# Kernel optimization log

Measured on AMD Instinct MI355X. Metric: run time of the kernel, lower is better.

The kernel has to match this reference:

```python
import jax, jax.numpy as jnp
import numpy as np

B, S, H, E = 8, 512, 1024, 8
T = B * S            # total tokens
CAP = T // E         # capacity, capacity_factor = 1.0


def _moe(x, wg, ew1, eb1, ew2, eb2):
    # x: [T, H] tokens; top-1 gating with capacity, DeepSpeed-style dispatch/combine
    gates = jax.nn.softmax(x @ wg)                      # [T, E]
    idx = jnp.argmax(gates, axis=-1)                    # [T]
    mask1 = jax.nn.one_hot(idx, E, dtype=x.dtype)       # [T, E]
    locations = jnp.cumsum(mask1, axis=0) - 1.0         # position within expert queue
    mask1 = mask1 * (locations < CAP).astype(x.dtype)   # drop overflow tokens
    gates1 = jnp.sum(gates * mask1, axis=-1)            # [T] combine weight
    locs = jnp.sum(locations * mask1, axis=-1).astype(jnp.int32)  # [T]
    loc_oh = jax.nn.one_hot(locs, CAP, dtype=x.dtype)   # [T, C]
    combine = gates1[:, None, None] * mask1[:, :, None] * loc_oh[:, None, :]  # [T,E,C]
    dispatch = (combine > 0).astype(x.dtype)            # [T, E, C]
    xd = jnp.einsum('sec,sm->ecm', dispatch, x)         # gather tokens per expert
    h = jnp.einsum('ecm,emn->ecn', xd, ew1) + eb1[:, None, :]
    h = jnp.einsum('ecn,enp->ecp', h, ew2) + eb2[:, None, :]
    return jnp.einsum('sec,ecm->sm', combine, h)        # scatter back, weighted


def setup_inputs() -> dict:
    key = jax.random.key(0)
    ks = jax.random.split(key, 16)
    w = lambda k, shape: jax.random.normal(k, shape, jnp.float32) * 0.02
    return {
        'x': jax.random.normal(ks[0], (B, S, H), jnp.float32),
        'y': jax.random.randint(ks[1], (B,), 0, H),
        'w1': w(ks[2], (H, H)), 'b1': jnp.zeros((H,), jnp.float32),
        'w2': w(ks[3], (H, H)), 'b2': jnp.zeros((H,), jnp.float32),
        'w3': w(ks[4], (H, H)), 'b3': jnp.zeros((H,), jnp.float32),
        'wg1': w(ks[5], (H, E)),
        'e1_w1': w(ks[6], (E, H, H)), 'e1_b1': jnp.zeros((E, H), jnp.float32),
        'e1_w2': w(ks[7], (E, H, H)), 'e1_b2': jnp.zeros((E, H), jnp.float32),
        'wg2': w(ks[8], (H, E)),
        'e2_w1': w(ks[9], (E, H, H)), 'e2_b1': jnp.zeros((E, H), jnp.float32),
        'e2_w2': w(ks[10], (E, H, H)), 'e2_b2': jnp.zeros((E, H), jnp.float32),
    }


def reference(x, y, w1, b1, w2, b2, w3, b3, wg1, e1_w1, e1_b1, e1_w2, e1_b2,
              wg2, e2_w1, e2_b1, e2_w2, e2_b2):
    xf = x.reshape(-1, H)                               # [T, H]
    hidden = xf @ w1 + b1
    out = _moe(hidden, wg1, e1_w1, e1_b1, e1_w2, e1_b2)
    out = out @ w2 + b2
    out = _moe(out, wg2, e2_w1, e2_b1, e2_w2, e2_b2)
    out = out @ w3 + b3
    hidden = hidden + out
    sent = hidden.reshape(B, S, H).mean(axis=1)         # [B, H] logits
    logp = jax.nn.log_softmax(sent, axis=-1)
    return -jnp.mean(logp[jnp.arange(B), y])
```

## Files before the change

### kernel.cpp

```cpp
#include <hip/hip_runtime.h>

#define TOK 4096
#define HID 1024
#define NEXP 8
#define CAP 512
#define WSZ 1048576

typedef _Float16 f16;
typedef f16 f16x8 __attribute__((ext_vector_type(8)));
typedef f16 f16x4 __attribute__((ext_vector_type(4)));
typedef f16 f16x2 __attribute__((ext_vector_type(2)));
typedef float f32x4 __attribute__((ext_vector_type(4)));

typedef const __attribute__((address_space(1))) void gvoid;
typedef __attribute__((address_space(3))) void lvoid;

__device__ __forceinline__ void gld16(const void* g, void* l) {
  __builtin_amdgcn_global_load_lds((gvoid*)g, (lvoid*)l, 16, 0, 0);
}

template<int MODE>
__global__ __launch_bounds__(512, 1) void gemm_h(
    const f16* __restrict__ A, const f16* __restrict__ Bt,
    const float* __restrict__ bias, f16* __restrict__ C,
    const int* __restrict__ rowmap, const float* __restrict__ gmax,
    int rowsPerExpert, long bStride, int biasStride)
{
  __shared__ f16 As[2][128 * 64];
  __shared__ f16 Bs[2][128 * 64];
  const int tid = threadIdx.x;
  const int w = tid >> 6, l = tid & 63;
  const int wr = w >> 2, wc = w & 3;

  const int orig = blockIdx.x;
  const int sw = (orig & 7) * 32 + (orig >> 3);
  const int bx = sw & 7, by = sw >> 3;
  const int e = (by * 128) / rowsPerExpert;

  const int lr = l >> 3;
  const int chunkSw = ((l & 7) ^ lr) * 8;

  const f16* pst[4];
  if (w < 4) {
    #pragma unroll
    for (int i = 0; i < 4; ++i) {
      int r = by * 128 + w * 32 + i * 8 + lr;
      long tok = r;
      if (MODE == 1) { int t = rowmap[r]; tok = (t < 0) ? (long)TOK : (long)t; }
      pst[i] = A + tok * HID + chunkSw;
    }
  } else {
    #pragma unroll
    for (int i = 0; i < 4; ++i)
      pst[i] = Bt + (size_t)e * bStride
             + (size_t)(bx * 128 + (w - 4) * 32 + i * 8 + lr) * HID + chunkSw;
  }

  f32x4 acc[4][2];
  #pragma unroll
  for (int i = 0; i < 4; ++i)
    #pragma unroll
    for (int j = 0; j < 2; ++j) acc[i][j] = (f32x4){0.f, 0.f, 0.f, 0.f};

  const int g = l >> 4, c = l & 15, sa = c & 7;

  {
    f16* db = (w < 4) ? &As[0][(w * 32) * 64] : &Bs[0][((w - 4) * 32) * 64];
    #pragma unroll
    for (int i = 0; i < 4; ++i) gld16(pst[i], db + i * 8 * 64);
  }

  int cur = 0;
  for (int t = 0; t < 15; ++t) {
    {
      const int k0 = (t + 1) * 64;
      f16* db = (w < 4) ? &As[cur ^ 1][(w * 32) * 64]
                        : &Bs[cur ^ 1][((w - 4) * 32) * 64];
      #pragma unroll
      for (int i = 0; i < 4; ++i) gld16(pst[i] + k0, db + i * 8 * 64);
    }
    asm volatile("s_waitcnt vmcnt(4)" ::: "memory");
    asm volatile("s_barrier" ::: "memory");
    __builtin_amdgcn_s_setprio(1);
    #pragma unroll
    for (int h = 0; h < 2; ++h) {
      const int q = ((h * 4 + g) ^ sa) * 8;
      f16x8 af[4], bf[2];
      #pragma unroll
      for (int mi = 0; mi < 4; ++mi)
        af[mi] = *(const f16x8*)&As[cur][(wr * 64 + mi * 16 + c) * 64 + q];
      #pragma unroll
      for (int ni = 0; ni < 2; ++ni)
        bf[ni] = *(const f16x8*)&Bs[cur][(wc * 32 + ni * 16 + c) * 64 + q];
      #pragma unroll
      for (int mi = 0; mi < 4; ++mi)
        #pragma unroll
        for (int ni = 0; ni < 2; ++ni)
          acc[mi][ni] = __builtin_amdgcn_mfma_f32_16x16x32_f16(
              af[mi], bf[ni], acc[mi][ni], 0, 0, 0);
    }
    __builtin_amdgcn_s_setprio(0);
    asm volatile("s_barrier" ::: "memory");
    cur ^= 1;
  }
  asm volatile("s_waitcnt vmcnt(0)" ::: "memory");
  asm volatile("s_barrier" ::: "memory");
  #pragma unroll
  for (int h = 0; h < 2; ++h) {
    const int q = ((h * 4 + g) ^ sa) * 8;
    f16x8 af[4], bf[2];
    #pragma unroll
    for (int mi = 0; mi < 4; ++mi)
      af[mi] = *(const f16x8*)&As[cur][(wr * 64 + mi * 16 + c) * 64 + q];
    #pragma unroll
    for (int ni = 0; ni < 2; ++ni)
      bf[ni] = *(const f16x8*)&Bs[cur][(wc * 32 + ni * 16 + c) * 64 + q];
    #pragma unroll
    for (int mi = 0; mi < 4; ++mi)
      #pragma unroll
      for (int ni = 0; ni < 2; ++ni)
        acc[mi][ni] = __builtin_amdgcn_mfma_f32_16x16x32_f16(
            af[mi], bf[ni], acc[mi][ni], 0, 0, 0);
  }

  int tk[4][4];
  float gv[4][4];
  if (MODE == 2) {
    #pragma unroll
    for (int mi = 0; mi < 4; ++mi)
      #pragma unroll
      for (int rr = 0; rr < 4; ++rr) {
        int r = by * 128 + wr * 64 + mi * 16 + g * 4 + rr;
        int t = rowmap[r];
        tk[mi][rr] = t;
        gv[mi][rr] = (t >= 0) ? gmax[t] : 0.f;
      }
  }
  #pragma unroll
  for (int ni = 0; ni < 2; ++ni) {
    const int col = bx * 128 + wc * 32 + ni * 16 + c;
    const float bv = bias[(size_t)e * biasStride + col];
    #pragma unroll
    for (int mi = 0; mi < 4; ++mi) {
      #pragma unroll
      for (int rr = 0; rr < 4; ++rr) {
        const float v = acc[mi][ni][rr] + bv;
        if (MODE == 2) {
          if (tk[mi][rr] >= 0)
            C[(size_t)tk[mi][rr] * HID + col] = (f16)(v * gv[mi][rr]);
        } else {
          const int row = by * 128 + wr * 64 + mi * 16 + g * 4 + rr;
          C[(size_t)row * HID + col] = (f16)v;
        }
      }
    }
  }
}

__global__ __launch_bounds__(256, 8) void tcast(
    const float* __restrict__ w1, const float* __restrict__ w2,
    const float* __restrict__ w3,
    const float* __restrict__ g1a, const float* __restrict__ g1b,
    const float* __restrict__ g2a, const float* __restrict__ g2b,
    f16* __restrict__ dst)
{
  __shared__ float t[64][65];
  const int z = blockIdx.z;
  const float* src; int zl = 0;
  if (z == 0) src = w1;
  else if (z == 1) src = w2;
  else if (z == 2) src = w3;
  else if (z < 11) { src = g1a; zl = z - 3; }
  else if (z < 19) { src = g1b; zl = z - 11; }
  else if (z < 27) { src = g2a; zl = z - 19; }
  else             { src = g2b; zl = z - 27; }
  src += (size_t)zl * WSZ;
  f16* d = dst + (size_t)z * WSZ;

  const int tid = threadIdx.x;
  const int kb = blockIdx.y * 64, nb = blockIdx.x * 64;
  const int rr = tid >> 4, c4 = (tid & 15) * 4;
  float4 v[4];
  #pragma unroll
  for (int p = 0; p < 4; ++p)
    v[p] = *(const float4*)&src[(size_t)(kb + p * 16 + rr) * HID + nb + c4];
  #pragma unroll
  for (int p = 0; p < 4; ++p) {
    t[p * 16 + rr][c4 + 0] = v[p].x;
    t[p * 16 + rr][c4 + 1] = v[p].y;
    t[p * 16 + rr][c4 + 2] = v[p].z;
    t[p * 16 + rr][c4 + 3] = v[p].w;
  }
  __syncthreads();
  #pragma unroll
  for (int half = 0; half < 2; ++half) {
    const int p = half * 256 + tid;
    const int n = p >> 3, kc = p & 7;
    f16x8 o;
    #pragma unroll
    for (int j = 0; j < 8; ++j) o[j] = (f16)t[kc * 8 + j][n];
    *(f16x8*)&d[(size_t)(nb + n) * HID + kb + kc * 8] = o;
  }
}

__global__ void prep(const float* __restrict__ x, f16* __restrict__ X0,
                     f16* __restrict__ c1, f16* __restrict__ c2,
                     f16* __restrict__ p1, f16* __restrict__ p2) {
  const size_t i = (size_t)blockIdx.x * 256 + threadIdx.x;
  float4 v = *(const float4*)&x[i * 4];
  f16x4 o = {(f16)v.x, (f16)v.y, (f16)v.z, (f16)v.w};
  *(f16x4*)&X0[i * 4] = o;
  const f16x8 zz = {0, 0, 0, 0, 0, 0, 0, 0};
  if (i < 524288) { ((f16x8*)c1)[i] = zz; ((f16x8*)c2)[i] = zz; }
  if (i < 128)    { ((f16x8*)p1)[i] = zz; ((f16x8*)p2)[i] = zz; }
}

__global__ __launch_bounds__(256) void gate_kernel(
    const f16* __restrict__ act, const float* __restrict__ wg,
    int* __restrict__ idx, float* __restrict__ gmax)
{
  const int tid = threadIdx.x;
  const int tok = blockIdx.x * 8 + (tid >> 5);
  const int sl = tid & 31;
  const f16* row = act + (size_t)tok * HID + sl * 32;
  float xv[32];
  #pragma unroll
  for (int v = 0; v < 4; ++v) {
    f16x8 hv = *(const f16x8*)(row + v * 8);
    #pragma unroll
    for (int j = 0; j < 8; ++j) xv[v * 8 + j] = (float)hv[j];
  }
  float p[NEXP];
  #pragma unroll
  for (int e = 0; e < NEXP; ++e) p[e] = 0.f;
  const float* wr_ = wg + (size_t)(sl * 32) * NEXP;
  #pragma unroll
  for (int j = 0; j < 32; ++j) {
    #pragma unroll
    for (int e = 0; e < NEXP; ++e) p[e] += xv[j] * wr_[j * NEXP + e];
  }
  #pragma unroll
  for (int m = 1; m < 32; m <<= 1) {
    #pragma unroll
    for (int e = 0; e < NEXP; ++e) p[e] += __shfl_xor(p[e], m, 64);
  }
  if (sl == 0) {
    float mx = p[0]; int am = 0;
    #pragma unroll
    for (int e = 1; e < NEXP; ++e)
      if (p[e] > mx) { mx = p[e]; am = e; }
    float s = 0.f;
    #pragma unroll
    for (int e = 0; e < NEXP; ++e) s += expf(p[e] - mx);
    idx[tok] = am;
    gmax[tok] = 1.f / s;
  }
}

__global__ __launch_bounds__(512) void scan_kernel(
    const int* __restrict__ idx, int* __restrict__ rowmap)
{
  __shared__ int sidx[TOK];
  const int tid = threadIdx.x;
  for (int i = tid; i < TOK; i += 512) sidx[i] = idx[i];
  for (int i = tid; i < NEXP * CAP; i += 512) rowmap[i] = -1;
  __syncthreads();
  const int wave = tid >> 6, lane = tid & 63;
  int running = 0;
  for (int ch = 0; ch < TOK / 64; ++ch) {
    int t = ch * 64 + lane;
    bool flag = (sidx[t] == wave);
    unsigned long long m = __ballot(flag);
    int pos = running + __popcll(m & ((1ull << lane) - 1ull));
    if (flag && pos < CAP) rowmap[wave * CAP + pos] = t;
    running += __popcll(m);
  }
}

__global__ __launch_bounds__(256) void mean1_kernel(
    const f16* __restrict__ a, const f16* __restrict__ c,
    float* __restrict__ partial)
{
  const int h2 = blockIdx.x * 256 + threadIdx.x;
  const int b = blockIdx.y, sc = blockIdx.z;
  const f16x2* pa = (const f16x2*)(a + ((size_t)b * 512 + sc * 32) * HID) + h2;
  const f16x2* pc = (const f16x2*)(c + ((size_t)b * 512 + sc * 32) * HID) + h2;
  float a0 = 0.f, a1 = 0.f;
  #pragma unroll 4
  for (int s = 0; s < 32; ++s) {
    f16x2 va = pa[(size_t)s * 512];
    f16x2 vc = pc[(size_t)s * 512];
    a0 += (float)va[0] + (float)vc[0];
    a1 += (float)va[1] + (float)vc[1];
  }
  float* o = partial + ((size_t)sc * 8 + b) * HID;
  o[h2 * 2]     = a0;
  o[h2 * 2 + 1] = a1;
}

__global__ __launch_bounds__(256) void mean2_kernel(
    const float* __restrict__ partial, float* __restrict__ sent)
{
  const int h2 = blockIdx.x * 256 + threadIdx.x;
  const int b = blockIdx.y;
  float a0 = 0.f, a1 = 0.f;
  #pragma unroll
  for (int sc = 0; sc < 16; ++sc) {
    const float* p = partial + ((size_t)sc * 8 + b) * HID + h2 * 2;
    a0 += p[0]; a1 += p[1];
  }
  sent[b * HID + h2 * 2]     = a0 * (1.f / 512.f);
  sent[b * HID + h2 * 2 + 1] = a1 * (1.f / 512.f);
}

__global__ __launch_bounds__(1024) void loss_kernel(
    const float* __restrict__ sent, const int* __restrict__ y,
    float* __restrict__ out)
{
  __shared__ float red[1024];
  float loss = 0.0f;
  for (int b = 0; b < 8; ++b) {
    float v = sent[b * HID + threadIdx.x];
    red[threadIdx.x] = v;
    __syncthreads();
    for (int s = 512; s > 0; s >>= 1) {
      if (threadIdx.x < s)
        red[threadIdx.x] = fmaxf(red[threadIdx.x], red[threadIdx.x + s]);
      __syncthreads();
    }
    float m = red[0];
    __syncthreads();
    red[threadIdx.x] = expf(v - m);
    __syncthreads();
    for (int s = 512; s > 0; s >>= 1) {
      if (threadIdx.x < s) red[threadIdx.x] += red[threadIdx.x + s];
      __syncthreads();
    }
    if (threadIdx.x == 0) {
      float lse = m + logf(red[0]);
      loss += -(sent[b * HID + y[b]] - lse);
    }
    __syncthreads();
  }
  if (threadIdx.x == 0) out[0] = loss * (1.0f / 8.0f);
}

extern "C" void kernel_launch(void* const* d_in, const int* in_sizes, int n_in,
                              void* d_out, int out_size, void* d_ws, size_t ws_size,
                              hipStream_t stream)
{
  const float* x    = (const float*)d_in[0];
  const int*   y    = (const int*)d_in[1];
  const float* w1   = (const float*)d_in[2];
  const float* b1   = (const float*)d_in[3];
  const float* w2   = (const float*)d_in[4];
  const float* b2   = (const float*)d_in[5];
  const float* w3   = (const float*)d_in[6];
  const float* b3   = (const float*)d_in[7];
  const float* wg1  = (const float*)d_in[8];
  const float* e1w1 = (const float*)d_in[9];
  const float* e1b1 = (const float*)d_in[10];
  const float* e1w2 = (const float*)d_in[11];
  const float* e1b2 = (const float*)d_in[12];
  const float* wg2  = (const float*)d_in[13];
  const float* e2w1 = (const float*)d_in[14];
  const float* e2b1 = (const float*)d_in[15];
  const float* e2w2 = (const float*)d_in[16];
  const float* e2b2 = (const float*)d_in[17];

  f16* WT = (f16*)d_ws;
  f16* X0 = WT + (size_t)35 * WSZ;
  f16* H  = X0 + (size_t)TOK * HID;
  f16* EA = H + (size_t)(TOK + 1) * HID;
  f16* C1 = EA + (size_t)TOK * HID;
  f16* M1 = C1 + (size_t)TOK * HID;
  f16* C2 = M1 + (size_t)(TOK + 1) * HID;
  f16* O  = C2 + (size_t)TOK * HID;
  float* gmax  = (float*)(O + (size_t)TOK * HID);
  int* idx     = (int*)(gmax + TOK);
  int* rowmap  = idx + TOK;
  float* sent  = (float*)(rowmap + TOK);
  float* partial = sent + 8 * HID;

  prep<<<4096, 256, 0, stream>>>(x, X0, C1, C2,
                                 H + (size_t)TOK * HID, M1 + (size_t)TOK * HID);
  tcast<<<dim3(16, 16, 35), 256, 0, stream>>>(w1, w2, w3, e1w1, e1w2, e2w1, e2w2, WT);

  gemm_h<0><<<256, 512, 0, stream>>>(X0, WT, b1, H, nullptr, nullptr, TOK, 0, 0);

  gate_kernel<<<512, 256, 0, stream>>>(H, wg1, idx, gmax);
  scan_kernel<<<1, 512, 0, stream>>>(idx, rowmap);
  gemm_h<1><<<256, 512, 0, stream>>>(H,  WT + (size_t)3 * WSZ,  e1b1, EA, rowmap, nullptr, CAP, WSZ, HID);
  gemm_h<2><<<256, 512, 0, stream>>>(EA, WT + (size_t)11 * WSZ, e1b2, C1, rowmap, gmax,    CAP, WSZ, HID);

  gemm_h<0><<<256, 512, 0, stream>>>(C1, WT + (size_t)1 * WSZ, b2, M1, nullptr, nullptr, TOK, 0, 0);

  gate_kernel<<<512, 256, 0, stream>>>(M1, wg2, idx, gmax);
  scan_kernel<<<1, 512, 0, stream>>>(idx, rowmap);
  gemm_h<1><<<256, 512, 0, stream>>>(M1, WT + (size_t)19 * WSZ, e2b1, EA, rowmap, nullptr, CAP, WSZ, HID);
  gemm_h<2><<<256, 512, 0, stream>>>(EA, WT + (size_t)27 * WSZ, e2b2, C2, rowmap, gmax,    CAP, WSZ, HID);

  gemm_h<0><<<256, 512, 0, stream>>>(C2, WT + (size_t)2 * WSZ, b3, O, nullptr, nullptr, TOK, 0, 0);

  mean1_kernel<<<dim3(2, 8, 16), 256, 0, stream>>>(H, O, partial);
  mean2_kernel<<<dim3(2, 8), 256, 0, stream>>>(partial, sent);
  loss_kernel<<<1, 1024, 0, stream>>>(sent, y, (float*)d_out);
}
```

Measured before the change: 229.0 us.

## Halve GEMM workgroup to 4 waves with 64x64 warp tiles; batch tcast tiles

The GEMM now runs 4 waves per 128x128 tile instead of 8. Each wave computes a 64x64 sub-tile (4x4 MFMA accumulators) and loads both A and B slices, and launch bounds allow 2 blocks per CU. The goal is more MFMA work per LDS fragment load and better overlap across two co-resident blocks, at the cost of higher register pressure and fewer waves per block. The weight transpose-cast kernel now processes four 64-row K tiles per block, loading them all up front, which cuts block count and increases memory-level parallelism per thread.

```diff
diff --git a/kernel.cpp b/kernel.cpp
--- a/kernel.cpp
+++ b/kernel.cpp
@@ -20,7 +20,7 @@
 }
 
 template<int MODE>
-__global__ __launch_bounds__(512, 1) void gemm_h(
+__global__ __launch_bounds__(256, 2) void gemm_h(
     const f16* __restrict__ A, const f16* __restrict__ Bt,
     const float* __restrict__ bias, f16* __restrict__ C,
     const int* __restrict__ rowmap, const float* __restrict__ gmax,
@@ -30,7 +30,7 @@
   __shared__ f16 Bs[2][128 * 64];
   const int tid = threadIdx.x;
   const int w = tid >> 6, l = tid & 63;
-  const int wr = w >> 2, wc = w & 3;
+  const int wr = w >> 1, wc = w & 1;
 
   const int orig = blockIdx.x;
   const int sw = (orig & 7) * 32 + (orig >> 3);
@@ -40,62 +40,62 @@
   const int lr = l >> 3;
   const int chunkSw = ((l & 7) ^ lr) * 8;
 
-  const f16* pst[4];
-  if (w < 4) {
-    #pragma unroll
-    for (int i = 0; i < 4; ++i) {
-      int r = by * 128 + w * 32 + i * 8 + lr;
-      long tok = r;
-      if (MODE == 1) { int t = rowmap[r]; tok = (t < 0) ? (long)TOK : (long)t; }
-      pst[i] = A + tok * HID + chunkSw;
-    }
-  } else {
-    #pragma unroll
-    for (int i = 0; i < 4; ++i)
-      pst[i] = Bt + (size_t)e * bStride
-             + (size_t)(bx * 128 + (w - 4) * 32 + i * 8 + lr) * HID + chunkSw;
-  }
-
-  f32x4 acc[4][2];
+  const f16* pa[4];
+  #pragma unroll
+  for (int i = 0; i < 4; ++i) {
+    int r = by * 128 + w * 32 + i * 8 + lr;
+    long tok = r;
+    if (MODE == 1) { int t = rowmap[r]; tok = (t < 0) ? (long)TOK : (long)t; }
+    pa[i] = A + tok * HID + chunkSw;
+  }
+  const f16* pb = Bt + (size_t)e * bStride
+                + (size_t)(bx * 128 + w * 32 + lr) * HID + chunkSw;
+
+  f32x4 acc[4][4];
   #pragma unroll
   for (int i = 0; i < 4; ++i)
     #pragma unroll
-    for (int j = 0; j < 2; ++j) acc[i][j] = (f32x4){0.f, 0.f, 0.f, 0.f};
+    for (int j = 0; j < 4; ++j) acc[i][j] = (f32x4){0.f, 0.f, 0.f, 0.f};
 
   const int g = l >> 4, c = l & 15, sa = c & 7;
 
   {
-    f16* db = (w < 4) ? &As[0][(w * 32) * 64] : &Bs[0][((w - 4) * 32) * 64];
-    #pragma unroll
-    for (int i = 0; i < 4; ++i) gld16(pst[i], db + i * 8 * 64);
+    f16* ab = &As[0][(w * 32) * 64];
+    f16* bb = &Bs[0][(w * 32) * 64];
+    #pragma unroll
+    for (int i = 0; i < 4; ++i) gld16(pa[i], ab + i * 8 * 64);
+    #pragma unroll
+    for (int i = 0; i < 4; ++i) gld16(pb + (size_t)(i * 8) * HID, bb + i * 8 * 64);
   }
 
   int cur = 0;
   for (int t = 0; t < 15; ++t) {
     {
       const int k0 = (t + 1) * 64;
-      f16* db = (w < 4) ? &As[cur ^ 1][(w * 32) * 64]
-                        : &Bs[cur ^ 1][((w - 4) * 32) * 64];
-      #pragma unroll
-      for (int i = 0; i < 4; ++i) gld16(pst[i] + k0, db + i * 8 * 64);
-    }
-    asm volatile("s_waitcnt vmcnt(4)" ::: "memory");
+      f16* ab = &As[cur ^ 1][(w * 32) * 64];
+      f16* bb = &Bs[cur ^ 1][(w * 32) * 64];
+      #pragma unroll
+      for (int i = 0; i < 4; ++i) gld16(pa[i] + k0, ab + i * 8 * 64);
+      #pragma unroll
+      for (int i = 0; i < 4; ++i) gld16(pb + (size_t)(i * 8) * HID + k0, bb + i * 8 * 64);
+    }
+    asm volatile("s_waitcnt vmcnt(8)" ::: "memory");
     asm volatile("s_barrier" ::: "memory");
     __builtin_amdgcn_s_setprio(1);
     #pragma unroll
     for (int h = 0; h < 2; ++h) {
       const int q = ((h * 4 + g) ^ sa) * 8;
-      f16x8 af[4], bf[2];
+      f16x8 af[4], bf[4];
       #pragma unroll
       for (int mi = 0; mi < 4; ++mi)
         af[mi] = *(const f16x8*)&As[cur][(wr * 64 + mi * 16 + c) * 64 + q];
       #pragma unroll
-      for (int ni = 0; ni < 2; ++ni)
-        bf[ni] = *(const f16x8*)&Bs[cur][(wc * 32 + ni * 16 + c) * 64 + q];
+      for (int ni = 0; ni < 4; ++ni)
+        bf[ni] = *(const f16x8*)&Bs[cur][(wc * 64 + ni * 16 + c) * 64 + q];
       #pragma unroll
       for (int mi = 0; mi < 4; ++mi)
         #pragma unroll
-        for (int ni = 0; ni < 2; ++ni)
+        for (int ni = 0; ni < 4; ++ni)
           acc[mi][ni] = __builtin_amdgcn_mfma_f32_16x16x32_f16(
               af[mi], bf[ni], acc[mi][ni], 0, 0, 0);
     }
@@ -105,23 +105,25 @@
   }
   asm volatile("s_waitcnt vmcnt(0)" ::: "memory");
   asm volatile("s_barrier" ::: "memory");
+  __builtin_amdgcn_s_setprio(1);
   #pragma unroll
   for (int h = 0; h < 2; ++h) {
     const int q = ((h * 4 + g) ^ sa) * 8;
-    f16x8 af[4], bf[2];
+    f16x8 af[4], bf[4];
     #pragma unroll
     for (int mi = 0; mi < 4; ++mi)
       af[mi] = *(const f16x8*)&As[cur][(wr * 64 + mi * 16 + c) * 64 + q];
     #pragma unroll
-    for (int ni = 0; ni < 2; ++ni)
-      bf[ni] = *(const f16x8*)&Bs[cur][(wc * 32 + ni * 16 + c) * 64 + q];
+    for (int ni = 0; ni < 4; ++ni)
+      bf[ni] = *(const f16x8*)&Bs[cur][(wc * 64 + ni * 16 + c) * 64 + q];
     #pragma unroll
     for (int mi = 0; mi < 4; ++mi)
       #pragma unroll
-      for (int ni = 0; ni < 2; ++ni)
+      for (int ni = 0; ni < 4; ++ni)
         acc[mi][ni] = __builtin_amdgcn_mfma_f32_16x16x32_f16(
             af[mi], bf[ni], acc[mi][ni], 0, 0, 0);
   }
+  __builtin_amdgcn_s_setprio(0);
 
   int tk[4][4];
   float gv[4][4];
@@ -137,8 +139,8 @@
       }
   }
   #pragma unroll
-  for (int ni = 0; ni < 2; ++ni) {
-    const int col = bx * 128 + wc * 32 + ni * 16 + c;
+  for (int ni = 0; ni < 4; ++ni) {
+    const int col = bx * 128 + wc * 64 + ni * 16 + c;
     const float bv = bias[(size_t)e * biasStride + col];
     #pragma unroll
     for (int mi = 0; mi < 4; ++mi) {
@@ -157,7 +159,7 @@
   }
 }
 
-__global__ __launch_bounds__(256, 8) void tcast(
+__global__ __launch_bounds__(256, 4) void tcast(
     const float* __restrict__ w1, const float* __restrict__ w2,
     const float* __restrict__ w3,
     const float* __restrict__ g1a, const float* __restrict__ g1b,
@@ -178,28 +180,36 @@
   f16* d = dst + (size_t)z * WSZ;
 
   const int tid = threadIdx.x;
-  const int kb = blockIdx.y * 64, nb = blockIdx.x * 64;
+  const int kb4 = blockIdx.y * 256, nb = blockIdx.x * 64;
   const int rr = tid >> 4, c4 = (tid & 15) * 4;
-  float4 v[4];
-  #pragma unroll
-  for (int p = 0; p < 4; ++p)
-    v[p] = *(const float4*)&src[(size_t)(kb + p * 16 + rr) * HID + nb + c4];
-  #pragma unroll
-  for (int p = 0; p < 4; ++p) {
-    t[p * 16 + rr][c4 + 0] = v[p].x;
-    t[p * 16 + rr][c4 + 1] = v[p].y;
-    t[p * 16 + rr][c4 + 2] = v[p].z;
-    t[p * 16 + rr][c4 + 3] = v[p].w;
-  }
-  __syncthreads();
-  #pragma unroll
-  for (int half = 0; half < 2; ++half) {
-    const int p = half * 256 + tid;
-    const int n = p >> 3, kc = p & 7;
-    f16x8 o;
-    #pragma unroll
-    for (int j = 0; j < 8; ++j) o[j] = (f16)t[kc * 8 + j][n];
-    *(f16x8*)&d[(size_t)(nb + n) * HID + kb + kc * 8] = o;
+
+  float4 v[4][4];
+  #pragma unroll
+  for (int tt = 0; tt < 4; ++tt)
+    #pragma unroll
+    for (int p = 0; p < 4; ++p)
+      v[tt][p] = *(const float4*)&src[(size_t)(kb4 + tt * 64 + p * 16 + rr) * HID + nb + c4];
+
+  #pragma unroll
+  for (int tt = 0; tt < 4; ++tt) {
+    if (tt) __syncthreads();
+    #pragma unroll
+    for (int p = 0; p < 4; ++p) {
+      t[p * 16 + rr][c4 + 0] = v[tt][p].x;
+      t[p * 16 + rr][c4 + 1] = v[tt][p].y;
+      t[p * 16 + rr][c4 + 2] = v[tt][p].z;
+      t[p * 16 + rr][c4 + 3] = v[tt][p].w;
+    }
+    __syncthreads();
+    #pragma unroll
+    for (int half = 0; half < 2; ++half) {
+      const int p = half * 256 + tid;
+      const int n = p >> 3, kc = p & 7;
+      f16x8 o;
+      #pragma unroll
+      for (int j = 0; j < 8; ++j) o[j] = (f16)t[kc * 8 + j][n];
+      *(f16x8*)&d[(size_t)(nb + n) * HID + kb4 + tt * 64 + kc * 8] = o;
+    }
   }
 }
 
@@ -384,23 +394,23 @@
 
   prep<<<4096, 256, 0, stream>>>(x, X0, C1, C2,
                                  H + (size_t)TOK * HID, M1 + (size_t)TOK * HID);
-  tcast<<<dim3(16, 16, 35), 256, 0, stream>>>(w1, w2, w3, e1w1, e1w2, e2w1, e2w2, WT);
-
-  gemm_h<0><<<256, 512, 0, stream>>>(X0, WT, b1, H, nullptr, nullptr, TOK, 0, 0);
+  tcast<<<dim3(16, 4, 35), 256, 0, stream>>>(w1, w2, w3, e1w1, e1w2, e2w1, e2w2, WT);
+
+  gemm_h<0><<<256, 256, 0, stream>>>(X0, WT, b1, H, nullptr, nullptr, TOK, 0, 0);
 
   gate_kernel<<<512, 256, 0, stream>>>(H, wg1, idx, gmax);
   scan_kernel<<<1, 512, 0, stream>>>(idx, rowmap);
-  gemm_h<1><<<256, 512, 0, stream>>>(H,  WT + (size_t)3 * WSZ,  e1b1, EA, rowmap, nullptr, CAP, WSZ, HID);
-  gemm_h<2><<<256, 512, 0, stream>>>(EA, WT + (size_t)11 * WSZ, e1b2, C1, rowmap, gmax,    CAP, WSZ, HID);
-
-  gemm_h<0><<<256, 512, 0, stream>>>(C1, WT + (size_t)1 * WSZ, b2, M1, nullptr, nullptr, TOK, 0, 0);
+  gemm_h<1><<<256, 256, 0, stream>>>(H,  WT + (size_t)3 * WSZ,  e1b1, EA, rowmap, nullptr, CAP, WSZ, HID);
+  gemm_h<2><<<256, 256, 0, stream>>>(EA, WT + (size_t)11 * WSZ, e1b2, C1, rowmap, gmax,    CAP, WSZ, HID);
+
+  gemm_h<0><<<256, 256, 0, stream>>>(C1, WT + (size_t)1 * WSZ, b2, M1, nullptr, nullptr, TOK, 0, 0);
 
   gate_kernel<<<512, 256, 0, stream>>>(M1, wg2, idx, gmax);
   scan_kernel<<<1, 512, 0, stream>>>(idx, rowmap);
-  gemm_h<1><<<256, 512, 0, stream>>>(M1, WT + (size_t)19 * WSZ, e2b1, EA, rowmap, nullptr, CAP, WSZ, HID);
-  gemm_h<2><<<256, 512, 0, stream>>>(EA, WT + (size_t)27 * WSZ, e2b2, C2, rowmap, gmax,    CAP, WSZ, HID);
-
-  gemm_h<0><<<256, 512, 0, stream>>>(C2, WT + (size_t)2 * WSZ, b3, O, nullptr, nullptr, TOK, 0, 0);
+  gemm_h<1><<<256, 256, 0, stream>>>(M1, WT + (size_t)19 * WSZ, e2b1, EA, rowmap, nullptr, CAP, WSZ, HID);
+  gemm_h<2><<<256, 256, 0, stream>>>(EA, WT + (size_t)27 * WSZ, e2b2, C2, rowmap, gmax,    CAP, WSZ, HID);
+
+  gemm_h<0><<<256, 256, 0, stream>>>(C2, WT + (size_t)2 * WSZ, b3, O, nullptr, nullptr, TOK, 0, 0);
 
   mean1_kernel<<<dim3(2, 8, 16), 256, 0, stream>>>(H, O, partial);
   mean2_kernel<<<dim3(2, 8), 256, 0, stream>>>(partial, sent);
```

Measured after the change: 277.3 us. 21.1% more time.

## Overlap expert weight transpose-casts with earlier GEMMs via extra blocks

Applied to the files above, without the earlier changes.

The large up-front transpose/cast of the 32 expert weight matrices is split across the first four GEMM launches. Each of those launches gets extra blocks beyond the 256 GEMM tiles, and these blocks transpose and cast the weights needed by a later GEMM. The aim is to fill idle compute units during the 256-block GEMMs (one block per CU) and to take the large serial tcast launch off the critical path. Shared memory is unified into one raw buffer. Extra setprio is added around the tail MFMA block, and the weights are still converted before their first use.

```diff
diff --git a/kernel.cpp b/kernel.cpp
--- a/kernel.cpp
+++ b/kernel.cpp
@@ -20,15 +20,52 @@
 }
 
 template<int MODE>
-__global__ __launch_bounds__(512, 1) void gemm_h(
+__global__ __launch_bounds__(512, 1) void gemm_fused(
     const f16* __restrict__ A, const f16* __restrict__ Bt,
     const float* __restrict__ bias, f16* __restrict__ C,
     const int* __restrict__ rowmap, const float* __restrict__ gmax,
-    int rowsPerExpert, long bStride, int biasStride)
-{
-  __shared__ f16 As[2][128 * 64];
-  __shared__ f16 Bs[2][128 * 64];
+    int rowsPerExpert, long bStride, int biasStride,
+    const float* __restrict__ tsrc, f16* __restrict__ tdst, int nGemm)
+{
+  __shared__ __align__(16) unsigned char smem[65536];
   const int tid = threadIdx.x;
+
+  if ((int)blockIdx.x >= nGemm) {
+    float (*t)[65] = (float (*)[65])smem;
+    const int tb = blockIdx.x - nGemm;
+    const int mat = tb >> 7, t7 = tb & 127;
+    const int nb = (t7 & 7) * 128, kb = (t7 >> 3) * 64;
+    const float* src = tsrc + (size_t)mat * WSZ;
+    f16* d = tdst + (size_t)mat * WSZ;
+    const int half = tid >> 8, tl = tid & 255;
+    const int rr = tl >> 4, c4 = (tl & 15) * 4;
+    float (*th)[65] = t + half * 64;
+    float4 v[4];
+    #pragma unroll
+    for (int p = 0; p < 4; ++p)
+      v[p] = *(const float4*)&src[(size_t)(kb + p * 16 + rr) * HID + nb + half * 64 + c4];
+    #pragma unroll
+    for (int p = 0; p < 4; ++p) {
+      th[p * 16 + rr][c4 + 0] = v[p].x;
+      th[p * 16 + rr][c4 + 1] = v[p].y;
+      th[p * 16 + rr][c4 + 2] = v[p].z;
+      th[p * 16 + rr][c4 + 3] = v[p].w;
+    }
+    __syncthreads();
+    #pragma unroll
+    for (int it = 0; it < 2; ++it) {
+      const int p = it * 256 + tl;
+      const int n = p >> 3, kc = p & 7;
+      f16x8 o;
+      #pragma unroll
+      for (int j = 0; j < 8; ++j) o[j] = (f16)th[kc * 8 + j][n];
+      *(f16x8*)&d[(size_t)(nb + half * 64 + n) * HID + kb + kc * 8] = o;
+    }
+    return;
+  }
+
+  f16* As0 = (f16*)smem;
+  f16* Bs0 = (f16*)(smem + 32768);
   const int w = tid >> 6, l = tid & 63;
   const int wr = w >> 2, wc = w & 3;
 
@@ -65,7 +102,7 @@
   const int g = l >> 4, c = l & 15, sa = c & 7;
 
   {
-    f16* db = (w < 4) ? &As[0][(w * 32) * 64] : &Bs[0][((w - 4) * 32) * 64];
+    f16* db = (w < 4) ? As0 + (w * 32) * 64 : Bs0 + ((w - 4) * 32) * 64;
     #pragma unroll
     for (int i = 0; i < 4; ++i) gld16(pst[i], db + i * 8 * 64);
   }
@@ -74,8 +111,8 @@
   for (int t = 0; t < 15; ++t) {
     {
       const int k0 = (t + 1) * 64;
-      f16* db = (w < 4) ? &As[cur ^ 1][(w * 32) * 64]
-                        : &Bs[cur ^ 1][((w - 4) * 32) * 64];
+      f16* db = (w < 4) ? As0 + ((cur ^ 1) * 8192) + (w * 32) * 64
+                        : Bs0 + ((cur ^ 1) * 8192) + ((w - 4) * 32) * 64;
       #pragma unroll
       for (int i = 0; i < 4; ++i) gld16(pst[i] + k0, db + i * 8 * 64);
     }
@@ -88,10 +125,10 @@
       f16x8 af[4], bf[2];
       #pragma unroll
       for (int mi = 0; mi < 4; ++mi)
-        af[mi] = *(const f16x8*)&As[cur][(wr * 64 + mi * 16 + c) * 64 + q];
+        af[mi] = *(const f16x8*)&As0[cur * 8192 + (wr * 64 + mi * 16 + c) * 64 + q];
       #pragma unroll
       for (int ni = 0; ni < 2; ++ni)
-        bf[ni] = *(const f16x8*)&Bs[cur][(wc * 32 + ni * 16 + c) * 64 + q];
+        bf[ni] = *(const f16x8*)&Bs0[cur * 8192 + (wc * 32 + ni * 16 + c) * 64 + q];
       #pragma unroll
       for (int mi = 0; mi < 4; ++mi)
         #pragma unroll
@@ -105,16 +142,17 @@
   }
   asm volatile("s_waitcnt vmcnt(0)" ::: "memory");
   asm volatile("s_barrier" ::: "memory");
+  __builtin_amdgcn_s_setprio(1);
   #pragma unroll
   for (int h = 0; h < 2; ++h) {
     const int q = ((h * 4 + g) ^ sa) * 8;
     f16x8 af[4], bf[2];
     #pragma unroll
     for (int mi = 0; mi < 4; ++mi)
-      af[mi] = *(const f16x8*)&As[cur][(wr * 64 + mi * 16 + c) * 64 + q];
+      af[mi] = *(const f16x8*)&As0[cur * 8192 + (wr * 64 + mi * 16 + c) * 64 + q];
     #pragma unroll
     for (int ni = 0; ni < 2; ++ni)
-      bf[ni] = *(const f16x8*)&Bs[cur][(wc * 32 + ni * 16 + c) * 64 + q];
+      bf[ni] = *(const f16x8*)&Bs0[cur * 8192 + (wc * 32 + ni * 16 + c) * 64 + q];
     #pragma unroll
     for (int mi = 0; mi < 4; ++mi)
       #pragma unroll
@@ -122,6 +160,7 @@
         acc[mi][ni] = __builtin_amdgcn_mfma_f32_16x16x32_f16(
             af[mi], bf[ni], acc[mi][ni], 0, 0, 0);
   }
+  __builtin_amdgcn_s_setprio(0);
 
   int tk[4][4];
   float gv[4][4];
@@ -157,26 +196,14 @@
   }
 }
 
-__global__ __launch_bounds__(256, 8) void tcast(
+__global__ __launch_bounds__(256, 8) void tcast3(
     const float* __restrict__ w1, const float* __restrict__ w2,
-    const float* __restrict__ w3,
-    const float* __restrict__ g1a, const float* __restrict__ g1b,
-    const float* __restrict__ g2a, const float* __restrict__ g2b,
-    f16* __restrict__ dst)
+    const float* __restrict__ w3, f16* __restrict__ dst)
 {
   __shared__ float t[64][65];
   const int z = blockIdx.z;
-  const float* src; int zl = 0;
-  if (z == 0) src = w1;
-  else if (z == 1) src = w2;
-  else if (z == 2) src = w3;
-  else if (z < 11) { src = g1a; zl = z - 3; }
-  else if (z < 19) { src = g1b; zl = z - 11; }
-  else if (z < 27) { src = g2a; zl = z - 19; }
-  else             { src = g2b; zl = z - 27; }
-  src += (size_t)zl * WSZ;
+  const float* src = (z == 0) ? w1 : (z == 1) ? w2 : w3;
   f16* d = dst + (size_t)z * WSZ;
-
   const int tid = threadIdx.x;
   const int kb = blockIdx.y * 64, nb = blockIdx.x * 64;
   const int rr = tid >> 4, c4 = (tid & 15) * 4;
@@ -382,25 +409,41 @@
   float* sent  = (float*)(rowmap + TOK);
   float* partial = sent + 8 * HID;
 
+  f16* WTe1a = WT + (size_t)3 * WSZ;
+  f16* WTe1b = WT + (size_t)11 * WSZ;
+  f16* WTe2a = WT + (size_t)19 * WSZ;
+  f16* WTe2b = WT + (size_t)27 * WSZ;
+
+  const int FUSED = 256 + 8 * 128;
+
   prep<<<4096, 256, 0, stream>>>(x, X0, C1, C2,
                                  H + (size_t)TOK * HID, M1 + (size_t)TOK * HID);
-  tcast<<<dim3(16, 16, 35), 256, 0, stream>>>(w1, w2, w3, e1w1, e1w2, e2w1, e2w2, WT);
-
-  gemm_h<0><<<256, 512, 0, stream>>>(X0, WT, b1, H, nullptr, nullptr, TOK, 0, 0);
+  tcast3<<<dim3(16, 16, 3), 256, 0, stream>>>(w1, w2, w3, WT);
+
+  gemm_fused<0><<<FUSED, 512, 0, stream>>>(X0, WT, b1, H, nullptr, nullptr,
+                                           TOK, 0, 0, e1w1, WTe1a, 256);
 
   gate_kernel<<<512, 256, 0, stream>>>(H, wg1, idx, gmax);
   scan_kernel<<<1, 512, 0, stream>>>(idx, rowmap);
-  gemm_h<1><<<256, 512, 0, stream>>>(H,  WT + (size_t)3 * WSZ,  e1b1, EA, rowmap, nullptr, CAP, WSZ, HID);
-  gemm_h<2><<<256, 512, 0, stream>>>(EA, WT + (size_t)11 * WSZ, e1b2, C1, rowmap, gmax,    CAP, WSZ, HID);
-
-  gemm_h<0><<<256, 512, 0, stream>>>(C1, WT + (size_t)1 * WSZ, b2, M1, nullptr, nullptr, TOK, 0, 0);
+  gemm_fused<1><<<FUSED, 512, 0, stream>>>(H, WTe1a, e1b1, EA, rowmap, nullptr,
+                                           CAP, WSZ, HID, e1w2, WTe1b, 256);
+  gemm_fused<2><<<FUSED, 512, 0, stream>>>(EA, WTe1b, e1b2, C1, rowmap, gmax,
+                                           CAP, WSZ, HID, e2w1, WTe2a, 256);
+
+  gemm_fused<0><<<FUSED, 512, 0, stream>>>(C1, WT + (size_t)1 * WSZ, b2, M1,
+                                           nullptr, nullptr, TOK, 0, 0,
+                                           e2w2, WTe2b, 256);
 
   gate_kernel<<<512, 256, 0, stream>>>(M1, wg2, idx, gmax);
   scan_kernel<<<1, 512, 0, stream>>>(idx, rowmap);
-  gemm_h<1><<<256, 512, 0, stream>>>(M1, WT + (size_t)19 * WSZ, e2b1, EA, rowmap, nullptr, CAP, WSZ, HID);
-  gemm_h<2><<<256, 512, 0, stream>>>(EA, WT + (size_t)27 * WSZ, e2b2, C2, rowmap, gmax,    CAP, WSZ, HID);
-
-  gemm_h<0><<<256, 512, 0, stream>>>(C2, WT + (size_t)2 * WSZ, b3, O, nullptr, nullptr, TOK, 0, 0);
+  gemm_fused<1><<<256, 512, 0, stream>>>(M1, WTe2a, e2b1, EA, rowmap, nullptr,
+                                         CAP, WSZ, HID, w1, WT, 256);
+  gemm_fused<2><<<256, 512, 0, stream>>>(EA, WTe2b, e2b2, C2, rowmap, gmax,
+                                         CAP, WSZ, HID, w1, WT, 256);
+
+  gemm_fused<0><<<256, 512, 0, stream>>>(C2, WT + (size_t)2 * WSZ, b3, O,
+                                         nullptr, nullptr, TOK, 0, 0,
+                                         w1, WT, 256);
 
   mean1_kernel<<<dim3(2, 8, 16), 256, 0, stream>>>(H, O, partial);
   mean2_kernel<<<dim3(2, 8), 256, 0, stream>>>(partial, sent);
```

New measurement: 223.4 us. 1.02x faster.
